# Performance work log

Measured on AMD Instinct MI355X. Metric: run time of the kernel, lower is better.

## Reference

```python
import jax, jax.numpy as jnp
import numpy as np
from jax import lax

N_LAYERS = 8
D_MODEL = 256
D_STATE = 64
EXPAND = 2
D_CONV = 4
HEADDIM = 32
D_INNER = EXPAND * D_MODEL            # 512
NHEADS = D_INNER // HEADDIM           # 16
CONV_DIM = D_INNER + 2 * D_STATE      # 640
D_IN_PROJ = 2 * D_INNER + 2 * D_STATE + NHEADS  # 1168
CHUNK = 64
B, L = 4, 2048
EPS = 1e-5


def setup_inputs() -> dict:
    key = jax.random.key(0)
    ks = iter(jax.random.split(key, 64))
    def rn(shape, s=1.0):
        return s * jax.random.normal(next(ks), shape, jnp.float32)
    inp = {"x": rn((B, L, D_MODEL))}
    for pre in ("fw", "bw"):
        inp[pre + "_ln_w"] = jnp.ones((N_LAYERS, D_MODEL), jnp.float32)
        inp[pre + "_ln_b"] = jnp.zeros((N_LAYERS, D_MODEL), jnp.float32)
        inp[pre + "_win"] = rn((N_LAYERS, D_IN_PROJ, D_MODEL), 0.05)
        inp[pre + "_convw"] = rn((N_LAYERS, CONV_DIM, D_CONV), 0.2)
        inp[pre + "_convb"] = jnp.zeros((N_LAYERS, CONV_DIM), jnp.float32)
        # A in [1, nheads] as in mamba2 init -> A_log = log(A)
        inp[pre + "_alog"] = jnp.log(jnp.tile(jnp.arange(1, NHEADS + 1, dtype=jnp.float32), (N_LAYERS, 1)))
        inp[pre + "_dtb"] = rn((N_LAYERS, NHEADS), 0.5)
        inp[pre + "_D"] = jnp.ones((N_LAYERS, NHEADS), jnp.float32)
        inp[pre + "_nw"] = jnp.ones((N_LAYERS, D_INNER), jnp.float32)
        inp[pre + "_wout"] = rn((N_LAYERS, D_MODEL, D_INNER), 0.05)
    inp["fusion_w"] = rn((D_MODEL, 2 * D_MODEL), 0.05)
    return inp


def _layernorm(x, w, b):
    mu = jnp.mean(x, -1, keepdims=True)
    v = jnp.mean(jnp.square(x - mu), -1, keepdims=True)
    return (x - mu) * lax.rsqrt(v + EPS) * w + b


def _ssd(xh, dt, A, Bm, Cm):
    # xh: (B,L,H,P)  dt: (B,L,H)  A: (H,)  Bm/Cm: (B,L,N).  Chunked SSD, chunk=CHUNK.
    Bb, Lq, H, P = xh.shape
    N = Bm.shape[-1]
    K = Lq // CHUNK
    xh = xh.reshape(Bb, K, CHUNK, H, P)
    dt = dt.reshape(Bb, K, CHUNK, H)
    Bm = Bm.reshape(Bb, K, CHUNK, N)
    Cm = Cm.reshape(Bb, K, CHUNK, N)
    dtA = dt * A                               # (B,K,C,H)
    cs = jnp.cumsum(dtA, axis=2)               # inclusive cumsum within chunk
    cs_t = cs.transpose(0, 1, 3, 2)            # (B,K,H,C)
    mask = jnp.tril(jnp.ones((CHUNK, CHUNK), bool))
    Lmat = jnp.where(mask, jnp.exp(cs_t[..., :, None] - cs_t[..., None, :]), 0.0)  # (B,K,H,C,C)
    CB = jnp.einsum('bkin,bkjn->bkij', Cm, Bm)  # (B,K,C,C)
    dt_t = dt.transpose(0, 1, 3, 2)             # (B,K,H,C)
    att = CB[:, :, None, :, :] * Lmat * dt_t[:, :, :, None, :]  # (B,K,H,C,C)
    y = jnp.einsum('bkhij,bkjhp->bkihp', att, xh)
    # chunk-local end states and cross-chunk recurrence
    decay_end = jnp.exp(cs_t[..., -1:] - cs_t)   # (B,K,H,C)
    w = decay_end * dt_t
    states = jnp.einsum('bkhj,bkjhp,bkjn->bkhpn', w, xh, Bm)  # (B,K,H,P,N)
    g = jnp.exp(cs_t[..., -1])                   # (B,K,H): total chunk decay
    def step(S, inputs):
        g_k, st_k = inputs
        return g_k[..., None, None] * S + st_k, S
    S0 = jnp.zeros((Bb, H, P, N), xh.dtype)
    _, Sprev = lax.scan(step, S0, (g.transpose(1, 0, 2), states.transpose(1, 0, 2, 3, 4)))
    # Sprev: (K,B,H,P,N) state at start of each chunk
    y_inter = jnp.einsum('bkin,kbhpn->bkihp', Cm, Sprev) * jnp.exp(cs)[..., None]
    return (y + y_inter).reshape(Bb, Lq, H, P)


def _mamba2(x, Win, convw, convb, A_log, dt_bias, Dp, norm_w, Wout):
    Bb, Lq, _ = x.shape
    zxbcdt = jnp.einsum('bld,ed->ble', x, Win)    # (B,L,D_IN_PROJ)
    z = zxbcdt[..., :D_INNER]
    xBC = zxbcdt[..., D_INNER:D_INNER + CONV_DIM]
    dt_raw = zxbcdt[..., D_INNER + CONV_DIM:]     # (B,L,H)
    # causal depthwise conv1d + silu
    xp = jnp.pad(xBC, ((0, 0), (D_CONV - 1, 0), (0, 0)))
    windows = jnp.stack([xp[:, k:k + Lq] for k in range(D_CONV)], axis=-1)  # (B,L,C,K)
    xc = jax.nn.silu(jnp.einsum('blck,ck->blc', windows, convw) + convb)
    xs = xc[..., :D_INNER].reshape(Bb, Lq, NHEADS, HEADDIM)
    Bm = xc[..., D_INNER:D_INNER + D_STATE]
    Cm = xc[..., D_INNER + D_STATE:]
    dt = jax.nn.softplus(dt_raw + dt_bias)
    A = -jnp.exp(A_log)
    y = _ssd(xs, dt, A, Bm, Cm) + Dp[None, None, :, None] * xs
    y = y.reshape(Bb, Lq, D_INNER)
    # gated RMSNorm (norm_before_gate=False): gate then normalize
    y = y * jax.nn.silu(z)
    y = y * lax.rsqrt(jnp.mean(jnp.square(y), -1, keepdims=True) + EPS) * norm_w
    return jnp.einsum('ble,de->bld', y, Wout)


def _run_stack(x, p):
    ln_w, ln_b, win, convw, convb, alog, dtb, Dp, nw, wout = p
    h = x
    for i in range(N_LAYERS):
        h = h + _mamba2(_layernorm(h, ln_w[i], ln_b[i]), win[i], convw[i], convb[i],
                        alog[i], dtb[i], Dp[i], nw[i], wout[i])
    return h


def reference(x,
              fw_ln_w, fw_ln_b, fw_win, fw_convw, fw_convb, fw_alog, fw_dtb, fw_D, fw_nw, fw_wout,
              bw_ln_w, bw_ln_b, bw_win, bw_convw, bw_convb, bw_alog, bw_dtb, bw_D, bw_nw, bw_wout,
              fusion_w):
    fw = (fw_ln_w, fw_ln_b, fw_win, fw_convw, fw_convb, fw_alog, fw_dtb, fw_D, fw_nw, fw_wout)
    bw = (bw_ln_w, bw_ln_b, bw_win, bw_convw, bw_convb, bw_alog, bw_dtb, bw_D, bw_nw, bw_wout)
    h_fwd = _run_stack(x, fw)
    h_bwd = jnp.flip(_run_stack(jnp.flip(x, 1), bw), 1)
    h = jnp.concatenate([h_fwd, h_bwd], axis=-1)      # (B,L,2D)
    return jnp.einsum('ble,de->bld', h, fusion_w)
```

## Files before the change

### kernel.cpp

```cpp
#include <hip/hip_runtime.h>
#include <math.h>


namespace {

constexpr int kL = 2048;
constexpr int kDM = 256;
constexpr int kDI = 512;
constexpr int kNH = 16;
constexpr int kDS = 64;
constexpr int kCDIM = 640;
constexpr int kDPROJ = 1168;
constexpr int kCH = 64;
constexpr int kKC = 32;
constexpr int kBB = 8;
constexpr int kRowsD = 4 * kL;
constexpr int kRows = kBB * kL;

typedef __bf16 bf16x8 __attribute__((ext_vector_type(8)));
typedef float f32x4 __attribute__((ext_vector_type(4)));
typedef unsigned short ushort;

union U16x8 {
  int4 v;
  ushort u[8];
  bf16x8 b;
};

__device__ __forceinline__ ushort f2b(float x) {
  union { float f; unsigned u; } c;
  c.f = x;
  unsigned r = c.u + 0x7fffu + ((c.u >> 16) & 1u);
  return (ushort)(r >> 16);
}
__device__ __forceinline__ float b2f(ushort u) {
  union { unsigned u; float f; } c;
  c.u = ((unsigned)u) << 16;
  return c.f;
}

__device__ __forceinline__ void gl_lds16(const void* g, void* l) {
  __builtin_amdgcn_global_load_lds(
      (const __attribute__((address_space(1))) unsigned int*)g,
      (__attribute__((address_space(3))) unsigned int*)l, 16, 0, 0);
}

constexpr int kQwin = 8 * kDPROJ * kDM / 4;
constexpr int kQwout = 8 * kDM * kDI / 4;
constexpr int kQfus = kDM * kDI / 4;
constexpr int kQtot = 2 * kQwin + 2 * kQwout + kQfus;

__global__ __launch_bounds__(256) void f2b_all_kernel(
    const float* __restrict__ s0, const float* __restrict__ s1,
    const float* __restrict__ s2, const float* __restrict__ s3,
    const float* __restrict__ s4, ushort* __restrict__ dst) {
  int i = blockIdx.x * 256 + threadIdx.x;
  if (i >= kQtot) return;
  const float* src;
  int off;
  if (i < kQwin) { src = s0; off = i; }
  else if (i < 2 * kQwin) { src = s1; off = i - kQwin; }
  else if (i < 2 * kQwin + kQwout) { src = s2; off = i - 2 * kQwin; }
  else if (i < 2 * kQwin + 2 * kQwout) { src = s3; off = i - 2 * kQwin - kQwout; }
  else { src = s4; off = i - 2 * kQwin - 2 * kQwout; }
  float4 v = *(const float4*)&src[(size_t)off * 4];
  ushort4 o = {f2b(v.x), f2b(v.y), f2b(v.z), f2b(v.w)};
  *(ushort4*)&dst[(size_t)i * 4] = o;
}

__global__ __launch_bounds__(256) void init_h_kernel(const float* __restrict__ x,
                                                     float* __restrict__ h) {
  int idx = blockIdx.x * 256 + threadIdx.x;
  if (idx >= 4 * kL * kDM) return;
  int d = idx & (kDM - 1);
  int l = (idx >> 8) & (kL - 1);
  int b = idx >> 19;
  float v = x[idx];
  h[idx] = v;
  h[((size_t)((4 + b) * kL + (kL - 1 - l))) * kDM + d] = v;
}

__global__ __launch_bounds__(256) void ln_kernel(const float* __restrict__ h,
                                                 const float* __restrict__ w0,
                                                 const float* __restrict__ b0,
                                                 const float* __restrict__ w1,
                                                 const float* __restrict__ b1,
                                                 ushort* __restrict__ xn) {
  int t = threadIdx.x;
  int lane = t & 63;
  int row = blockIdx.x * 4 + (t >> 6);
  int dir = (row >= kRowsD) ? 1 : 0;
  const float* w = dir ? w1 : w0;
  const float* b = dir ? b1 : b0;
  int e0 = lane * 4;
  float4 v = *(const float4*)&h[(size_t)row * kDM + e0];
  float s = v.x + v.y + v.z + v.w;
#pragma unroll
  for (int o = 32; o > 0; o >>= 1) s += __shfl_xor(s, o);
  float mu = s * (1.0f / kDM);
  float4 d = {v.x - mu, v.y - mu, v.z - mu, v.w - mu};
  float ss = d.x * d.x + d.y * d.y + d.z * d.z + d.w * d.w;
#pragma unroll
  for (int o = 32; o > 0; o >>= 1) ss += __shfl_xor(ss, o);
  float r = rsqrtf(ss * (1.0f / kDM) + 1e-5f);
  float4 wv = *(const float4*)&w[e0];
  float4 bv = *(const float4*)&b[e0];
  ushort4 o = {f2b(d.x * r * wv.x + bv.x), f2b(d.y * r * wv.y + bv.y),
               f2b(d.z * r * wv.z + bv.z), f2b(d.w * r * wv.w + bv.w)};
  *(ushort4*)&xn[(size_t)row * kDM + e0] = o;
}

__global__ __launch_bounds__(256) void gemm_bf16(const ushort* __restrict__ A,
                                                 const ushort* __restrict__ W0,
                                                 const ushort* __restrict__ W1,
                                                 ushort* __restrict__ C16,
                                                 float* __restrict__ dtraw, int Md,
                                                 int N, int K, int NT) {
  int dir = blockIdx.z;
  const ushort* W = dir ? W1 : W0;
  const ushort* Ab = A + (size_t)dir * Md * K;
  int wg = blockIdx.x;
  int chunk = gridDim.x >> 3;
  int swz = (wg & 7) * chunk + (wg >> 3);
  int m0 = (swz / NT) * 128;
  int n0 = (swz % NT) * 128;
  __shared__ __align__(16) ushort As[128 * 32];
  __shared__ __align__(16) ushort Ws[128 * 32];
  int tid = threadIdx.x;
  int lane = tid & 63;
  int wv = tid >> 6;
  int wr = (wv >> 1) * 64, wc = (wv & 1) * 64;
  int l16 = lane & 15, lk = lane >> 4;
  int rA = tid >> 2;
  int cA = (tid & 3) * 8;
  char* ldsA = (char*)As + wv * 1024;
  char* ldsB = (char*)Ws + wv * 1024;
  int rb0 = n0 + rA;       if (rb0 >= N) rb0 = N - 1;
  int rb1 = n0 + rA + 64;  if (rb1 >= N) rb1 = N - 1;

  f32x4 acc[4][4];
#pragma unroll
  for (int m = 0; m < 4; m++)
#pragma unroll
    for (int n = 0; n < 4; n++) acc[m][n] = {0.f, 0.f, 0.f, 0.f};

  for (int k0 = 0; k0 < K; k0 += 32) {
    gl_lds16(Ab + (size_t)(m0 + rA) * K + k0 + cA, ldsA);
    gl_lds16(Ab + (size_t)(m0 + rA + 64) * K + k0 + cA, ldsA + 4096);
    gl_lds16(W + (size_t)rb0 * K + k0 + cA, ldsB);
    gl_lds16(W + (size_t)rb1 * K + k0 + cA, ldsB + 4096);
    __syncthreads();
    bf16x8 a[4], b[4];
#pragma unroll
    for (int m = 0; m < 4; m++)
      a[m] = *(const bf16x8*)((const char*)As +
                              (((wr + m * 16 + l16) * 32 + lk * 8) << 1));
#pragma unroll
    for (int n = 0; n < 4; n++)
      b[n] = *(const bf16x8*)((const char*)Ws +
                              (((wc + n * 16 + l16) * 32 + lk * 8) << 1));
#pragma unroll
    for (int m = 0; m < 4; m++)
#pragma unroll
      for (int n = 0; n < 4; n++)
        acc[m][n] =
            __builtin_amdgcn_mfma_f32_16x16x32_bf16(a[m], b[n], acc[m][n], 0, 0, 0);
    __syncthreads();
  }
  ushort* Cb = C16 + (size_t)dir * Md * N;
  float* dtb = dtraw + (size_t)dir * Md * kNH;
#pragma unroll
  for (int m = 0; m < 4; m++) {
#pragma unroll
    for (int n = 0; n < 4; n++) {
      int col = n0 + wc + n * 16 + l16;
      if (col < N) {
#pragma unroll
        for (int r = 0; r < 4; r++) {
          int row = m0 + wr + m * 16 + lk * 4 + r;
          float v = acc[m][n][r];
          Cb[(size_t)row * N + col] = f2b(v);
          if (col >= 2 * kDI + 2 * kDS)
            dtb[(size_t)row * kNH + (col - (2 * kDI + 2 * kDS))] = v;
        }
      }
    }
  }
}

__global__ __launch_bounds__(256) void gemm_bf16_64(const ushort* __restrict__ A,
                                                    const ushort* __restrict__ W0,
                                                    const ushort* __restrict__ W1,
                                                    float* __restrict__ C, int Md,
                                                    int N, int K, int NT,
                                                    int accumulate) {
  int dir = blockIdx.z;
  const ushort* W = dir ? W1 : W0;
  const ushort* Ab = A + (size_t)dir * Md * K;
  float* Cb = C + (size_t)dir * Md * N;
  int wg = blockIdx.x;
  int chunk = gridDim.x >> 3;
  int swz = (wg & 7) * chunk + (wg >> 3);
  int m0 = (swz / NT) * 64;
  int n0 = (swz % NT) * 64;
  __shared__ __align__(16) ushort As[64 * 32];
  __shared__ __align__(16) ushort Ws[64 * 32];
  int tid = threadIdx.x;
  int lane = tid & 63;
  int wv = tid >> 6;
  int wr = (wv >> 1) * 32, wc = (wv & 1) * 32;
  int l16 = lane & 15, lk = lane >> 4;
  int rA = tid >> 2;
  int cA = (tid & 3) * 8;
  char* ldsA = (char*)As + wv * 1024;
  char* ldsB = (char*)Ws + wv * 1024;

  f32x4 acc[2][2];
#pragma unroll
  for (int m = 0; m < 2; m++)
#pragma unroll
    for (int n = 0; n < 2; n++) acc[m][n] = {0.f, 0.f, 0.f, 0.f};

  for (int k0 = 0; k0 < K; k0 += 32) {
    gl_lds16(Ab + (size_t)(m0 + rA) * K + k0 + cA, ldsA);
    gl_lds16(W + (size_t)(n0 + rA) * K + k0 + cA, ldsB);
    __syncthreads();
    bf16x8 a[2], b[2];
#pragma unroll
    for (int m = 0; m < 2; m++)
      a[m] = *(const bf16x8*)((const char*)As +
                              (((wr + m * 16 + l16) * 32 + lk * 8) << 1));
#pragma unroll
    for (int n = 0; n < 2; n++)
      b[n] = *(const bf16x8*)((const char*)Ws +
                              (((wc + n * 16 + l16) * 32 + lk * 8) << 1));
#pragma unroll
    for (int m = 0; m < 2; m++)
#pragma unroll
      for (int n = 0; n < 2; n++)
        acc[m][n] =
            __builtin_amdgcn_mfma_f32_16x16x32_bf16(a[m], b[n], acc[m][n], 0, 0, 0);
    __syncthreads();
  }
#pragma unroll
  for (int m = 0; m < 2; m++) {
#pragma unroll
    for (int n = 0; n < 2; n++) {
      int col = n0 + wc + n * 16 + l16;
#pragma unroll
      for (int r = 0; r < 4; r++) {
        int row = m0 + wr + m * 16 + lk * 4 + r;
        size_t idx = (size_t)row * N + col;
        float v = acc[m][n][r];
        if (accumulate) Cb[idx] += v;
        else Cb[idx] = v;
      }
    }
  }
}

constexpr int kConvBlocks = (kRows / 16) * (kCDIM / 8) / 256;

__global__ __launch_bounds__(256) void conv_cumsum_kernel(
    const ushort* __restrict__ zxb, const float* __restrict__ cw0,
    const float* __restrict__ cb0, const float* __restrict__ cw1,
    const float* __restrict__ cb1, ushort* __restrict__ xcb,
    const float* __restrict__ dtraw, const float* __restrict__ db0,
    const float* __restrict__ db1, const float* __restrict__ al0,
    const float* __restrict__ al1, float* __restrict__ dt,
    float* __restrict__ cs, float* __restrict__ g) {
  if ((int)blockIdx.x < kConvBlocks) {
    constexpr int kCG = kCDIM / 8;
    int idx = blockIdx.x * 256 + threadIdx.x;
    int c8 = (idx % kCG) * 8;
    int rt = idx / kCG;
    int bb = rt >> 7;
    int l0 = (rt & 127) << 4;
    int dir = bb >> 2;
    const float* cw = dir ? cw1 : cw0;
    const float* cb = dir ? cb1 : cb0;
    float wt[8][4];
#pragma unroll
    for (int c = 0; c < 8; c++) {
      float4 w = *(const float4*)&cw[(c8 + c) * 4];
      wt[c][0] = w.x; wt[c][1] = w.y; wt[c][2] = w.z; wt[c][3] = w.w;
    }
    float bias[8];
    {
      float4 b0 = *(const float4*)&cb[c8];
      float4 b1 = *(const float4*)&cb[c8 + 4];
      bias[0] = b0.x; bias[1] = b0.y; bias[2] = b0.z; bias[3] = b0.w;
      bias[4] = b1.x; bias[5] = b1.y; bias[6] = b1.z; bias[7] = b1.w;
    }
    const ushort* base = zxb + ((size_t)(bb * kL)) * kDPROJ + kDI + c8;
    float w0[8], w1[8], w2[8];
    if (l0 == 0) {
#pragma unroll
      for (int c = 0; c < 8; c++) { w0[c] = 0.f; w1[c] = 0.f; w2[c] = 0.f; }
    } else {
      U16x8 a, b, c;
      a.v = *(const int4*)(base + (size_t)(l0 - 3) * kDPROJ);
      b.v = *(const int4*)(base + (size_t)(l0 - 2) * kDPROJ);
      c.v = *(const int4*)(base + (size_t)(l0 - 1) * kDPROJ);
#pragma unroll
      for (int q = 0; q < 8; q++) {
        w0[q] = b2f(a.u[q]); w1[q] = b2f(b.u[q]); w2[q] = b2f(c.u[q]);
      }
    }
    ushort* outp = xcb + (size_t)(bb * kL + l0) * kCDIM + c8;
#pragma unroll
    for (int r = 0; r < 16; r++) {
      U16x8 cu;
      cu.v = *(const int4*)(base + (size_t)(l0 + r) * kDPROJ);
      U16x8 o;
#pragma unroll
      for (int c = 0; c < 8; c++) {
        float cf = b2f(cu.u[c]);
        float a = bias[c] + wt[c][0] * w0[c] + wt[c][1] * w1[c] + wt[c][2] * w2[c] +
                  wt[c][3] * cf;
        o.u[c] = f2b(a / (1.f + __expf(-a)));
        w0[c] = w1[c];
        w1[c] = w2[c];
        w2[c] = cf;
      }
      *(int4*)(outp + (size_t)r * kCDIM) = o.v;
    }
  } else {
    int t = threadIdx.x;
    int c = t & 63;
    int wid = ((int)blockIdx.x - kConvBlocks) * 4 + (t >> 6);
    int h = wid & (kNH - 1);
    int k = (wid >> 4) & (kKC - 1);
    int bb = wid >> 9;
    int dir = bb >> 2;
    int row = bb * kL + k * kCH + c;
    float x = dtraw[(size_t)row * kNH + h] + (dir ? db1 : db0)[h];
    float dtv = (x > 20.f) ? x : log1pf(expf(x));
    dt[(size_t)row * kNH + h] = dtv;
    float A = -__expf((dir ? al1 : al0)[h]);
    float s = dtv * A;
#pragma unroll
    for (int off = 1; off < 64; off <<= 1) {
      float u = __shfl_up(s, off);
      if (c >= off) s += u;
    }
    cs[(size_t)wid * kCH + c] = s;
    if (c == 63) g[wid] = __expf(s);
  }
}

__global__ __launch_bounds__(256) void states_kernel(const ushort* __restrict__ xcb,
                                                     const float* __restrict__ dt,
                                                     const float* __restrict__ cs,
                                                     ushort* __restrict__ states) {
  int bk = blockIdx.x;
  int k = bk & (kKC - 1);
  int bb = bk >> 5;
  __shared__ __align__(16) ushort Bstage[64][72];
  __shared__ __align__(16) ushort Bt[64][72];
  __shared__ __align__(16) ushort Ap[4][32][72];
  __shared__ float w_s[16][64];
  int t = threadIdx.x;
  int lane = t & 63, wv = t >> 6;
  size_t rowbase = (size_t)(bb * kL + k * kCH);
  {
    int j = t >> 2, n0 = (t & 3) * 16;
    const ushort* src = xcb + (rowbase + j) * kCDIM + kDI + n0;
    *(int4*)&Bstage[j][n0] = *(const int4*)src;
    *(int4*)&Bstage[j][n0 + 8] = *(const int4*)(src + 8);
  }
#pragma unroll
  for (int i = 0; i < 4; i++) {
    int e = t + i * 256;
    int h = e >> 6, c = e & 63;
    const float* csb = cs + ((size_t)bk * 16 + h) * kCH;
    w_s[h][c] = __expf(csb[63] - csb[c]) * dt[(rowbase + c) * kNH + h];
  }
  __syncthreads();
#pragma unroll
  for (int i = 0; i < 16; i++) {
    int e = t + i * 256;
    int j = e & 63, n = e >> 6;
    Bt[n][j] = Bstage[j][n];
  }
  __syncthreads();
  int l15 = lane & 15, lk8 = (lane >> 4) * 8;
  for (int hg = 0; hg < 4; hg++) {
    int h = hg * 4 + wv;
    float wl = w_s[h][lane];
    const ushort* xrow = xcb + (rowbase + lane) * kCDIM + h * 32;
#pragma unroll
    for (int q4 = 0; q4 < 4; q4++) {
      U16x8 v;
      v.v = *(const int4*)(xrow + q4 * 8);
#pragma unroll
      for (int q = 0; q < 8; q++)
        Ap[wv][q4 * 8 + q][lane] = f2b(b2f(v.u[q]) * wl);
    }
#pragma unroll
    for (int pt = 0; pt < 2; pt++) {
#pragma unroll
      for (int nt = 0; nt < 4; nt++) {
        f32x4 acc = {0.f, 0.f, 0.f, 0.f};
#pragma unroll
        for (int kt = 0; kt < 2; kt++) {
          bf16x8 a = *(const bf16x8*)&Ap[wv][pt * 16 + l15][kt * 32 + lk8];
          bf16x8 b = *(const bf16x8*)&Bt[nt * 16 + l15][kt * 32 + lk8];
          acc = __builtin_amdgcn_mfma_f32_16x16x32_bf16(a, b, acc, 0, 0, 0);
        }
        size_t base = ((size_t)bk * 16 + h) * 2048;
#pragma unroll
        for (int r = 0; r < 4; r++) {
          int p = pt * 16 + (lane >> 4) * 4 + r;
          states[base + p * 64 + nt * 16 + l15] = f2b(acc[r]);
        }
      }
    }
  }
}

__global__ __launch_bounds__(256) void scan_kernel(const ushort* __restrict__ st,
                                                   const float* __restrict__ g,
                                                   ushort* __restrict__ spbf) {
  int idx = blockIdx.x * 256 + threadIdx.x;
  if (idx >= kBB * kNH * 512) return;
  int pn4 = (idx & 511) * 4;
  int h = (idx >> 9) & (kNH - 1);
  int bb = idx >> 13;
  float S[4] = {0.f, 0.f, 0.f, 0.f};
  for (int k = 0; k < kKC; k++) {
    size_t off = (((size_t)(bb * kKC + k) * kNH + h) * 2048) + pn4;
    ushort4 so = {f2b(S[0]), f2b(S[1]), f2b(S[2]), f2b(S[3])};
    *(ushort4*)&spbf[off] = so;
    ushort4 sv = *(const ushort4*)&st[off];
    float gk = g[(bb * kKC + k) * kNH + h];
    S[0] = gk * S[0] + b2f(sv.x);
    S[1] = gk * S[1] + b2f(sv.y);
    S[2] = gk * S[2] + b2f(sv.z);
    S[3] = gk * S[3] + b2f(sv.w);
  }
}

__global__ __launch_bounds__(256) void y_kernel(const ushort* __restrict__ xcb,
                                                const float* __restrict__ dt,
                                                const float* __restrict__ cs,
                                                const ushort* __restrict__ spbf,
                                                const float* __restrict__ D0,
                                                const float* __restrict__ D1,
                                                ushort* __restrict__ y) {
  int bid = blockIdx.x;
  int hh = bid & 1;
  int bk = bid >> 1;
  int k = bk & (kKC - 1);
  int bb = bk >> 5;
  int dir = bb >> 2;
  __shared__ __align__(16) ushort Cls[64][72];
  __shared__ __align__(16) ushort Bls[64][72];
  __shared__ float CBT[64][67];
  __shared__ __align__(16) ushort xs_s[64][40];
  __shared__ __align__(16) ushort xsT[32][72];
  __shared__ __align__(16) ushort sp_s[32][72];
  __shared__ float cs_s[64], dt_s[64], ecs_s[64];
  int t = threadIdx.x, lane = t & 63, wv = t >> 6;
  int l15 = lane & 15, lk8 = (lane >> 4) * 8;
  size_t rowbase = (size_t)(bb * kL + k * kCH);
  {
    int j = t >> 2, n0 = (t & 3) * 16;
    const ushort* pB = xcb + (rowbase + j) * kCDIM + kDI;
    *(int4*)&Bls[j][n0] = *(const int4*)(pB + n0);
    *(int4*)&Bls[j][n0 + 8] = *(const int4*)(pB + n0 + 8);
    *(int4*)&Cls[j][n0] = *(const int4*)(pB + kDS + n0);
    *(int4*)&Cls[j][n0 + 8] = *(const int4*)(pB + kDS + n0 + 8);
  }
  __syncthreads();
  {
    int i0 = wv * 16;
#pragma unroll
    for (int jt = 0; jt < 4; jt++) {
      f32x4 acc = {0.f, 0.f, 0.f, 0.f};
#pragma unroll
      for (int kt = 0; kt < 2; kt++) {
        bf16x8 a = *(const bf16x8*)&Cls[i0 + l15][kt * 32 + lk8];
        bf16x8 b = *(const bf16x8*)&Bls[jt * 16 + l15][kt * 32 + lk8];
        acc = __builtin_amdgcn_mfma_f32_16x16x32_bf16(a, b, acc, 0, 0, 0);
      }
#pragma unroll
      for (int r = 0; r < 4; r++)
        CBT[jt * 16 + l15][i0 + (lane >> 4) * 4 + r] = acc[r];
    }
  }
  for (int hi = 0; hi < 8; hi++) {
    int h = hh * 8 + hi;
    int bkh = bk * 16 + h;
    float Dp = (dir ? D1 : D0)[h];
    __syncthreads();
    {
      int j = t >> 2, p0 = (t & 3) * 8;
      U16x8 v;
      v.v = *(const int4*)(xcb + (rowbase + j) * kCDIM + h * 32 + p0);
      *(int4*)&xs_s[j][p0] = v.v;
#pragma unroll
      for (int q = 0; q < 8; q++) xsT[p0 + q][j] = v.u[q];
      int4 s = *(const int4*)(spbf + (size_t)bkh * 2048 + t * 8);
      *(int4*)&sp_s[t >> 3][(t & 7) * 8] = s;
      if (t < 64) {
        float cv = cs[(size_t)bkh * kCH + t];
        cs_s[t] = cv;
        ecs_s[t] = __expf(cv);
        dt_s[t] = dt[(rowbase + t) * kNH + h];
      }
    }
    __syncthreads();
    int i0 = wv * 16;
    int ia = i0 + l15;
    float csi = cs_s[ia];
    U16x8 af[2];
#pragma unroll
    for (int kt = 0; kt < 2; kt++) {
#pragma unroll
      for (int q = 0; q < 8; q++) {
        int j = kt * 32 + lk8 + q;
        float v = 0.f;
        if (j <= ia) v = __expf(csi - cs_s[j]) * dt_s[j] * CBT[j][ia];
        af[kt].u[q] = f2b(v);
      }
    }
#pragma unroll
    for (int pt = 0; pt < 2; pt++) {
      f32x4 acc = {0.f, 0.f, 0.f, 0.f};
      f32x4 acc2 = {0.f, 0.f, 0.f, 0.f};
#pragma unroll
      for (int kt = 0; kt < 2; kt++) {
        bf16x8 bx = *(const bf16x8*)&xsT[pt * 16 + l15][kt * 32 + lk8];
        acc = __builtin_amdgcn_mfma_f32_16x16x32_bf16(af[kt].b, bx, acc, 0, 0, 0);
        bf16x8 ac = *(const bf16x8*)&Cls[i0 + l15][kt * 32 + lk8];
        bf16x8 bs = *(const bf16x8*)&sp_s[pt * 16 + l15][kt * 32 + lk8];
        acc2 = __builtin_amdgcn_mfma_f32_16x16x32_bf16(ac, bs, acc2, 0, 0, 0);
      }
#pragma unroll
      for (int r = 0; r < 4; r++) {
        int io = i0 + (lane >> 4) * 4 + r;
        int p = pt * 16 + l15;
        float xsv = b2f(xs_s[io][p]);
        float v = acc[r] + ecs_s[io] * acc2[r] + Dp * xsv;
        y[(rowbase + io) * kDI + h * 32 + p] = f2b(v);
      }
    }
  }
}

__global__ __launch_bounds__(256) void gate_norm_kernel(const ushort* __restrict__ zxb,
                                                        const float* __restrict__ nw0,
                                                        const float* __restrict__ nw1,
                                                        const ushort* __restrict__ y,
                                                        ushort* __restrict__ ybf) {
  int t = threadIdx.x;
  int lane = t & 63;
  int row = blockIdx.x * 4 + (t >> 6);
  int dir = (row >= kRowsD) ? 1 : 0;
  const float* nw = dir ? nw1 : nw0;
  int e0 = lane * 8;
  U16x8 zu, yu;
  zu.v = *(const int4*)(zxb + (size_t)row * kDPROJ + e0);
  yu.v = *(const int4*)(y + (size_t)row * kDI + e0);
  float v[8];
  float ss = 0.f;
#pragma unroll
  for (int q = 0; q < 8; q++) {
    float z = b2f(zu.u[q]);
    float gz = z / (1.f + __expf(-z));
    v[q] = b2f(yu.u[q]) * gz;
    ss += v[q] * v[q];
  }
#pragma unroll
  for (int o = 32; o > 0; o >>= 1) ss += __shfl_xor(ss, o);
  float scale = rsqrtf(ss * (1.0f / kDI) + 1e-5f);
  float4 n0 = *(const float4*)&nw[e0];
  float4 n1 = *(const float4*)&nw[e0 + 4];
  float na[8] = {n0.x, n0.y, n0.z, n0.w, n1.x, n1.y, n1.z, n1.w};
  U16x8 o;
#pragma unroll
  for (int q = 0; q < 8; q++) o.u[q] = f2b(v[q] * scale * na[q]);
  *(int4*)&ybf[(size_t)row * kDI + e0] = o.v;
}

__global__ __launch_bounds__(256) void concat_kernel(const float* __restrict__ h,
                                                     ushort* __restrict__ hcat) {
  int idx = blockIdx.x * 256 + threadIdx.x;
  if (idx >= 4 * kL * 2 * kDM) return;
  int e = idx & 511;
  int l = (idx >> 9) & (kL - 1);
  int b = idx >> 20;
  float v;
  if (e < kDM)
    v = h[((size_t)(b * kL + l)) * kDM + e];
  else
    v = h[((size_t)((4 + b) * kL + (kL - 1 - l))) * kDM + (e - kDM)];
  hcat[idx] = f2b(v);
}

}

extern "C" void kernel_launch(void* const* d_in, const int* in_sizes, int n_in,
                              void* d_out, int out_size, void* d_ws, size_t ws_size,
                              hipStream_t stream) {
  const float* x = (const float*)d_in[0];
  const float* fw_ln_w = (const float*)d_in[1];
  const float* fw_ln_b = (const float*)d_in[2];
  const float* fw_win = (const float*)d_in[3];
  const float* fw_convw = (const float*)d_in[4];
  const float* fw_convb = (const float*)d_in[5];
  const float* fw_alog = (const float*)d_in[6];
  const float* fw_dtb = (const float*)d_in[7];
  const float* fw_D = (const float*)d_in[8];
  const float* fw_nw = (const float*)d_in[9];
  const float* fw_wout = (const float*)d_in[10];
  const float* bw_ln_w = (const float*)d_in[11];
  const float* bw_ln_b = (const float*)d_in[12];
  const float* bw_win = (const float*)d_in[13];
  const float* bw_convw = (const float*)d_in[14];
  const float* bw_convb = (const float*)d_in[15];
  const float* bw_alog = (const float*)d_in[16];
  const float* bw_dtb = (const float*)d_in[17];
  const float* bw_D = (const float*)d_in[18];
  const float* bw_nw = (const float*)d_in[19];
  const float* bw_wout = (const float*)d_in[20];
  const float* fusion_w = (const float*)d_in[21];
  float* out = (float*)d_out;

  float* ws = (float*)d_ws;
  float* h = ws;
  float* dtraw = h + (size_t)kRows * kDM;
  float* dt = dtraw + (size_t)kRows * kNH;
  float* cs = dt + (size_t)kRows * kNH;
  float* g = cs + (size_t)kBB * kKC * kNH * kCH;
  ushort* zxb = (ushort*)(g + (size_t)kBB * kKC * kNH);
  ushort* xcb = zxb + (size_t)kRows * kDPROJ;
  ushort* states = xcb + (size_t)kRows * kCDIM;
  ushort* spbf = states + (size_t)kBB * kKC * kNH * 2048;
  ushort* ybuf = spbf + (size_t)kBB * kKC * kNH * 2048;
  ushort* xnbf = ybuf + (size_t)kRows * kDI;
  ushort* ybf = xnbf + (size_t)kRows * kDM;
  ushort* winbf = ybf + (size_t)kRows * kDI;
  ushort* woutbf = winbf + (size_t)2 * 8 * kDPROJ * kDM;
  ushort* fusbf = woutbf + (size_t)2 * 8 * kDM * kDI;
  ushort* hcatbf = xnbf;

  f2b_all_kernel<<<(kQtot + 255) / 256, 256, 0, stream>>>(fw_win, bw_win, fw_wout,
                                                          bw_wout, fusion_w, winbf);
  init_h_kernel<<<(4 * kL * kDM + 255) / 256, 256, 0, stream>>>(x, h);

  for (int i = 0; i < 8; i++) {
    const size_t oLN = (size_t)i * kDM;
    const size_t oCW = (size_t)i * kCDIM * 4;
    const size_t oCB = (size_t)i * kCDIM;
    const size_t oH = (size_t)i * kNH;
    const size_t oNW = (size_t)i * kDI;
    const ushort* win0 = winbf + (size_t)i * kDPROJ * kDM;
    const ushort* win1 = winbf + (size_t)(8 + i) * kDPROJ * kDM;
    const ushort* wout0 = woutbf + (size_t)i * kDM * kDI;
    const ushort* wout1 = woutbf + (size_t)(8 + i) * kDM * kDI;

    ln_kernel<<<kRows / 4, 256, 0, stream>>>(h, fw_ln_w + oLN, fw_ln_b + oLN,
                                             bw_ln_w + oLN, bw_ln_b + oLN, xnbf);
    {
      dim3 grid(10 * 64, 1, 2);
      gemm_bf16<<<grid, 256, 0, stream>>>(xnbf, win0, win1, zxb, dtraw, kRowsD,
                                          kDPROJ, kDM, 10);
    }
    {
      int cumsumBlocks = kBB * kKC * kNH / 4;
      conv_cumsum_kernel<<<kConvBlocks + cumsumBlocks, 256, 0, stream>>>(
          zxb, fw_convw + oCW, fw_convb + oCB, bw_convw + oCW, bw_convb + oCB, xcb,
          dtraw, fw_dtb + oH, bw_dtb + oH, fw_alog + oH, bw_alog + oH, dt, cs, g);
    }
    states_kernel<<<kBB * kKC, 256, 0, stream>>>(xcb, dt, cs, states);
    scan_kernel<<<(kBB * kNH * 512 + 255) / 256, 256, 0, stream>>>(states, g, spbf);
    y_kernel<<<kBB * kKC * 2, 256, 0, stream>>>(xcb, dt, cs, spbf, fw_D + oH,
                                                bw_D + oH, ybuf);
    gate_norm_kernel<<<kRows / 4, 256, 0, stream>>>(zxb, fw_nw + oNW, bw_nw + oNW,
                                                    ybuf, ybf);
    {
      dim3 grid(4 * 128, 1, 2);
      gemm_bf16_64<<<grid, 256, 0, stream>>>(ybf, wout0, wout1, h, kRowsD, kDM, kDI,
                                             4, 1);
    }
  }

  concat_kernel<<<(4 * kL * 2 * kDM + 255) / 256, 256, 0, stream>>>(h, hcatbf);
  {
    dim3 grid(4 * 128, 1, 1);
    gemm_bf16_64<<<grid, 256, 0, stream>>>(hcatbf, fusbf, fusbf, out, kRowsD, kDM,
                                           2 * kDM, 4, 0);
  }
}
```

Measured before the change: 954.4 us.

## Fuse gated RMSNorm into output projection GEMM prologue

```diff
diff --git a/kernel.cpp b/kernel.cpp
--- a/kernel.cpp
+++ b/kernel.cpp
@@ -188,16 +188,107 @@
   }
 }
 
+__global__ __launch_bounds__(256) void out_fused_kernel(
+    const ushort* __restrict__ zxb, const ushort* __restrict__ ybuf,
+    const float* __restrict__ nw0, const float* __restrict__ nw1,
+    const ushort* __restrict__ W0, const ushort* __restrict__ W1,
+    float* __restrict__ h) {
+  int dir = blockIdx.z;
+  const ushort* W = dir ? W1 : W0;
+  const float* nw = dir ? nw1 : nw0;
+  int m0 = blockIdx.x * 32;
+  size_t growbase = (size_t)dir * kRowsD + m0;
+  __shared__ __align__(16) ushort Als[32][520];
+  __shared__ __align__(16) ushort Wls[256 * 32];
+  int tid = threadIdx.x;
+  int lane = tid & 63, wv = tid >> 6;
+  int l16 = lane & 15, lk = lane >> 4;
+
+  {
+    int j = tid >> 3;
+    int c0 = (tid & 7) * 64;
+    const ushort* zp = zxb + (growbase + j) * kDPROJ + c0;
+    const ushort* yp = ybuf + (growbase + j) * kDI + c0;
+    float v[64];
+    float ss = 0.f;
+#pragma unroll
+    for (int q = 0; q < 8; q++) {
+      U16x8 zu, yu;
+      zu.v = *(const int4*)(zp + q * 8);
+      yu.v = *(const int4*)(yp + q * 8);
+#pragma unroll
+      for (int e = 0; e < 8; e++) {
+        float z = b2f(zu.u[e]);
+        float gz = z / (1.f + __expf(-z));
+        float val = b2f(yu.u[e]) * gz;
+        v[q * 8 + e] = val;
+        ss += val * val;
+      }
+    }
+#pragma unroll
+    for (int o = 1; o < 8; o <<= 1) ss += __shfl_xor(ss, o);
+    float scale = rsqrtf(ss * (1.0f / kDI) + 1e-5f);
+#pragma unroll
+    for (int q = 0; q < 8; q++) {
+      float4 na0 = *(const float4*)&nw[c0 + q * 8];
+      float4 na1 = *(const float4*)&nw[c0 + q * 8 + 4];
+      float na[8] = {na0.x, na0.y, na0.z, na0.w, na1.x, na1.y, na1.z, na1.w};
+      U16x8 o;
+#pragma unroll
+      for (int e = 0; e < 8; e++) o.u[e] = f2b(v[q * 8 + e] * scale * na[e]);
+      *(int4*)&Als[j][c0 + q * 8] = o.v;
+    }
+  }
+  __syncthreads();
+
+  f32x4 acc[2][4];
+#pragma unroll
+  for (int m = 0; m < 2; m++)
+#pragma unroll
+    for (int n = 0; n < 4; n++) acc[m][n] = {0.f, 0.f, 0.f, 0.f};
+
+  for (int k0 = 0; k0 < kDI; k0 += 32) {
+#pragma unroll
+    for (int q = 0; q < 4; q++)
+      gl_lds16(W + (size_t)(q * 64 + (tid >> 2)) * kDI + k0 + (tid & 3) * 8,
+               (char*)Wls + q * 4096 + wv * 1024);
+    __syncthreads();
+    bf16x8 a[2], b[4];
+#pragma unroll
+    for (int m = 0; m < 2; m++)
+      a[m] = *(const bf16x8*)&Als[m * 16 + l16][k0 + lk * 8];
+#pragma unroll
+    for (int n = 0; n < 4; n++)
+      b[n] = *(const bf16x8*)&Wls[(wv * 64 + n * 16 + l16) * 32 + lk * 8];
+#pragma unroll
+    for (int m = 0; m < 2; m++)
+#pragma unroll
+      for (int n = 0; n < 4; n++)
+        acc[m][n] =
+            __builtin_amdgcn_mfma_f32_16x16x32_bf16(a[m], b[n], acc[m][n], 0, 0, 0);
+    __syncthreads();
+  }
+#pragma unroll
+  for (int m = 0; m < 2; m++) {
+#pragma unroll
+    for (int n = 0; n < 4; n++) {
+      int col = wv * 64 + n * 16 + l16;
+#pragma unroll
+      for (int r = 0; r < 4; r++) {
+        size_t grow = growbase + m * 16 + lk * 4 + r;
+        h[grow * kDM + col] += acc[m][n][r];
+      }
+    }
+  }
+}
+
 __global__ __launch_bounds__(256) void gemm_bf16_64(const ushort* __restrict__ A,
                                                     const ushort* __restrict__ W0,
-                                                    const ushort* __restrict__ W1,
                                                     float* __restrict__ C, int Md,
-                                                    int N, int K, int NT,
-                                                    int accumulate) {
-  int dir = blockIdx.z;
-  const ushort* W = dir ? W1 : W0;
-  const ushort* Ab = A + (size_t)dir * Md * K;
-  float* Cb = C + (size_t)dir * Md * N;
+                                                    int N, int K, int NT) {
+  const ushort* W = W0;
+  const ushort* Ab = A;
+  float* Cb = C;
   int wg = blockIdx.x;
   int chunk = gridDim.x >> 3;
   int swz = (wg & 7) * chunk + (wg >> 3);
@@ -250,10 +341,7 @@
 #pragma unroll
       for (int r = 0; r < 4; r++) {
         int row = m0 + wr + m * 16 + lk * 4 + r;
-        size_t idx = (size_t)row * N + col;
-        float v = acc[m][n][r];
-        if (accumulate) Cb[idx] += v;
-        else Cb[idx] = v;
+        Cb[(size_t)row * N + col] = acc[m][n][r];
       }
     }
   }
@@ -549,41 +637,6 @@
   }
 }
 
-__global__ __launch_bounds__(256) void gate_norm_kernel(const ushort* __restrict__ zxb,
-                                                        const float* __restrict__ nw0,
-                                                        const float* __restrict__ nw1,
-                                                        const ushort* __restrict__ y,
-                                                        ushort* __restrict__ ybf) {
-  int t = threadIdx.x;
-  int lane = t & 63;
-  int row = blockIdx.x * 4 + (t >> 6);
-  int dir = (row >= kRowsD) ? 1 : 0;
-  const float* nw = dir ? nw1 : nw0;
-  int e0 = lane * 8;
-  U16x8 zu, yu;
-  zu.v = *(const int4*)(zxb + (size_t)row * kDPROJ + e0);
-  yu.v = *(const int4*)(y + (size_t)row * kDI + e0);
-  float v[8];
-  float ss = 0.f;
-#pragma unroll
-  for (int q = 0; q < 8; q++) {
-    float z = b2f(zu.u[q]);
-    float gz = z / (1.f + __expf(-z));
-    v[q] = b2f(yu.u[q]) * gz;
-    ss += v[q] * v[q];
-  }
-#pragma unroll
-  for (int o = 32; o > 0; o >>= 1) ss += __shfl_xor(ss, o);
-  float scale = rsqrtf(ss * (1.0f / kDI) + 1e-5f);
-  float4 n0 = *(const float4*)&nw[e0];
-  float4 n1 = *(const float4*)&nw[e0 + 4];
-  float na[8] = {n0.x, n0.y, n0.z, n0.w, n1.x, n1.y, n1.z, n1.w};
-  U16x8 o;
-#pragma unroll
-  for (int q = 0; q < 8; q++) o.u[q] = f2b(v[q] * scale * na[q]);
-  *(int4*)&ybf[(size_t)row * kDI + e0] = o.v;
-}
-
 __global__ __launch_bounds__(256) void concat_kernel(const float* __restrict__ h,
                                                      ushort* __restrict__ hcat) {
   int idx = blockIdx.x * 256 + threadIdx.x;
@@ -640,8 +693,7 @@
   ushort* spbf = states + (size_t)kBB * kKC * kNH * 2048;
   ushort* ybuf = spbf + (size_t)kBB * kKC * kNH * 2048;
   ushort* xnbf = ybuf + (size_t)kRows * kDI;
-  ushort* ybf = xnbf + (size_t)kRows * kDM;
-  ushort* winbf = ybf + (size_t)kRows * kDI;
+  ushort* winbf = xnbf + (size_t)kRows * kDM;
   ushort* woutbf = winbf + (size_t)2 * 8 * kDPROJ * kDM;
   ushort* fusbf = woutbf + (size_t)2 * 8 * kDM * kDI;
   ushort* hcatbf = xnbf;
@@ -678,19 +730,17 @@
     scan_kernel<<<(kBB * kNH * 512 + 255) / 256, 256, 0, stream>>>(states, g, spbf);
     y_kernel<<<kBB * kKC * 2, 256, 0, stream>>>(xcb, dt, cs, spbf, fw_D + oH,
                                                 bw_D + oH, ybuf);
-    gate_norm_kernel<<<kRows / 4, 256, 0, stream>>>(zxb, fw_nw + oNW, bw_nw + oNW,
-                                                    ybuf, ybf);
     {
-      dim3 grid(4 * 128, 1, 2);
-      gemm_bf16_64<<<grid, 256, 0, stream>>>(ybf, wout0, wout1, h, kRowsD, kDM, kDI,
-                                             4, 1);
+      dim3 grid(kRowsD / 32, 1, 2);
+      out_fused_kernel<<<grid, 256, 0, stream>>>(zxb, ybuf, fw_nw + oNW, bw_nw + oNW,
+                                                 wout0, wout1, h);
     }
   }
 
   concat_kernel<<<(4 * kL * 2 * kDM + 255) / 256, 256, 0, stream>>>(h, hcatbf);
   {
     dim3 grid(4 * 128, 1, 1);
-    gemm_bf16_64<<<grid, 256, 0, stream>>>(hcatbf, fusbf, fusbf, out, kRowsD, kDM,
-                                           2 * kDM, 4, 0);
-  }
-}
+    gemm_bf16_64<<<grid, 256, 0, stream>>>(hcatbf, fusbf, out, kRowsD, kDM,
+                                           2 * kDM, 4);
+  }
+}
```

After: 967.9 us. Within noise of the previous version (+1.4%).
